# Performance work log

Hardware: AMD Instinct MI355X
Metric: run time of the kernel (lower is better)

The kernel has to match this reference:

```python
import jax, jax.numpy as jnp
import numpy as np
from jax import lax


def _lstm_layer(x, h0, c0, W_ih, W_hh, b_ih, b_hh):
    # x: [B,T,I]; precompute input projection for all timesteps: [B,T,4H]
    xg = jnp.einsum('bti,gi->btg', x, W_ih) + b_ih

    def step(carry, xg_t):
        h, c = carry
        gates = xg_t + h @ W_hh.T + b_hh  # [B,4H]
        i, f, g, o = jnp.split(gates, 4, axis=-1)  # PyTorch LSTMCell gate order
        i = jax.nn.sigmoid(i)
        f = jax.nn.sigmoid(f)
        g = jnp.tanh(g)
        o = jax.nn.sigmoid(o)
        c = f * c + i * g
        h = o * jnp.tanh(c)
        return (h, c), h

    (h, c), ys = lax.scan(step, (h0, c0), jnp.swapaxes(xg, 0, 1))  # scan over T
    return jnp.swapaxes(ys, 0, 1), h, c  # [B,T,H], [B,H], [B,H]


def setup_inputs() -> dict:
    key = jax.random.key(0)
    ks = jax.random.split(key, 10)
    B, T, I, H = 128, 256, 256, 1024
    s = 0.02
    return {
        'x': jax.random.normal(ks[0], (B, T, I), jnp.float32),
        'hx0': jnp.zeros((2, B, H), jnp.float32),
        'cx0': jnp.zeros((2, B, H), jnp.float32),
        'W_ih0': jax.random.normal(ks[1], (4 * H, I), jnp.float32) * s,
        'W_hh0': jax.random.normal(ks[2], (4 * H, H), jnp.float32) * s,
        'b_ih0': jax.random.normal(ks[3], (4 * H,), jnp.float32) * s,
        'b_hh0': jax.random.normal(ks[4], (4 * H,), jnp.float32) * s,
        'W_ih1': jax.random.normal(ks[5], (4 * H, H), jnp.float32) * s,
        'W_hh1': jax.random.normal(ks[6], (4 * H, H), jnp.float32) * s,
        'b_ih1': jax.random.normal(ks[7], (4 * H,), jnp.float32) * s,
        'b_hh1': jax.random.normal(ks[8], (4 * H,), jnp.float32) * s,
    }


def reference(x, hx0, cx0, W_ih0, W_hh0, b_ih0, b_hh0, W_ih1, W_hh1, b_ih1, b_hh1):
    # Eval mode / variational_inference=False with dropout=0.0: masks are exact ones.
    x, h, c = _lstm_layer(x, hx0[0], cx0[0], W_ih0, W_hh0, b_ih0, b_hh0)
    x, h, c = _lstm_layer(x, hx0[1], cx0[1], W_ih1, W_hh1, b_ih1, b_hh1)
    return x, h, c
```

## Files before the change

kernel.cpp:

```cpp
#include <hip/hip_runtime.h>

typedef __attribute__((ext_vector_type(8))) short short8;
typedef __attribute__((ext_vector_type(4))) float f32x4;

#define DEV static __device__ __forceinline__

DEV unsigned short f2b(float f) {
    union { float f; unsigned u; } v; v.f = f;
    unsigned r = (v.u + 0x7FFFu + ((v.u >> 16) & 1u)) >> 16;
    return (unsigned short)r;
}
DEV float b2f(unsigned short s) {
    union { unsigned u; float f; } v; v.u = ((unsigned)s) << 16;
    return v.f;
}
DEV float sigm(float x) { return 1.0f / (1.0f + __expf(-x)); }


__global__ void k_f2b(const float* __restrict__ src, unsigned short* __restrict__ dst, int n4) {
    int i = blockIdx.x * blockDim.x + threadIdx.x;
    if (i < n4) {
        float4 v = ((const float4*)src)[i];
        ushort4 o;
        o.x = f2b(v.x); o.y = f2b(v.y); o.z = f2b(v.z); o.w = f2b(v.w);
        ((ushort4*)dst)[i] = o;
    }
}

__global__ void k_perm(const float* __restrict__ src, unsigned short* __restrict__ dst, int Kq) {
    int i = blockIdx.x * blockDim.x + threadIdx.x;
    int total = 4096 * Kq;
    if (i >= total) return;
    int rp = i / Kq, kq = i - rp * Kq;
    int j = rp >> 2, g = rp & 3;
    float4 v = ((const float4*)src)[(size_t)(g * 1024 + j) * Kq + kq];
    ushort4 o;
    o.x = f2b(v.x); o.y = f2b(v.y); o.z = f2b(v.z); o.w = f2b(v.w);
    ((ushort4*)dst)[(size_t)rp * Kq + kq] = o;
}

__global__ void k_bias(const float* __restrict__ bi0, const float* __restrict__ bh0,
                       const float* __restrict__ bi1, const float* __restrict__ bh1,
                       float* __restrict__ d0, float* __restrict__ d1) {
    int i = blockIdx.x * blockDim.x + threadIdx.x;
    if (i < 4096) {
        int j = i >> 2, g = i & 3, s = g * 1024 + j;
        d0[i] = bi0[s] + bh0[s];
        d1[i] = bi1[s] + bh1[s];
    }
}

__global__ void k_init(const float* __restrict__ hx, const float* __restrict__ cx,
                       unsigned* __restrict__ hB0, unsigned* __restrict__ hB1,
                       float* __restrict__ c0, float* __restrict__ c1) {
    int i = blockIdx.x * blockDim.x + threadIdx.x;
    if (i < 128 * 512) {
        int b = i >> 9, j = i & 511;
        const float* p0 = hx + (size_t)b * 1024 + j * 2;
        const float* p1 = hx + 131072 + (size_t)b * 1024 + j * 2;
        hB0[i] = (unsigned)f2b(p0[0]) | ((unsigned)f2b(p0[1]) << 16);
        hB1[i] = (unsigned)f2b(p1[0]) | ((unsigned)f2b(p1[1]) << 16);
        c0[i * 2] = cx[i * 2];
        c0[i * 2 + 1] = cx[i * 2 + 1];
        c1[i * 2] = cx[131072 + i * 2];
        c1[i * 2 + 1] = cx[131072 + i * 2 + 1];
    }
}

__global__ __launch_bounds__(256) void k_gemm(
    const unsigned short* __restrict__ A, const unsigned short* __restrict__ W,
    unsigned short* __restrict__ out, int K, int t0, int TC) {
    __shared__ unsigned short ldsA[128 * 40];
    __shared__ unsigned short ldsB[128 * 40];
    const int tid = threadIdx.x;
    const int w = tid >> 6, l = tid & 63;
    const int wm = w >> 1, wn = w & 1;
    const int bm = blockIdx.x, bn = blockIdx.y;
    const int lr = l & 15, lk = (l >> 4) * 8;

    const int row0 = tid >> 2, inb = (tid & 3) << 4;
    const int row1 = row0 + 64;
    const int v0 = bm * 128 + row0, v1 = bm * 128 + row1;
    const size_t ar0 = (size_t)((v0 / TC) * 256 + t0 + (v0 % TC));
    const size_t ar1 = (size_t)((v1 / TC) * 256 + t0 + (v1 % TC));
    const size_t br0 = (size_t)(bn * 128 + row0);
    const size_t br1 = (size_t)(bn * 128 + row1);

    f32x4 acc[4][4];
#pragma unroll
    for (int a = 0; a < 4; a++)
#pragma unroll
        for (int b = 0; b < 4; b++) acc[a][b] = (f32x4){0.f, 0.f, 0.f, 0.f};

    for (int ks = 0; ks < K; ks += 32) {
        uint4 a0 = *(const uint4*)((const char*)A + (ar0 * K + ks) * 2 + inb);
        uint4 a1 = *(const uint4*)((const char*)A + (ar1 * K + ks) * 2 + inb);
        uint4 b0 = *(const uint4*)((const char*)W + (br0 * K + ks) * 2 + inb);
        uint4 b1 = *(const uint4*)((const char*)W + (br1 * K + ks) * 2 + inb);
        *(uint4*)((char*)ldsA + row0 * 80 + inb) = a0;
        *(uint4*)((char*)ldsA + row1 * 80 + inb) = a1;
        *(uint4*)((char*)ldsB + row0 * 80 + inb) = b0;
        *(uint4*)((char*)ldsB + row1 * 80 + inb) = b1;
        __syncthreads();
        short8 af[4], bf[4];
#pragma unroll
        for (int mt = 0; mt < 4; mt++)
            af[mt] = *(const short8*)((const char*)ldsA + (wm * 64 + mt * 16 + lr) * 80 + lk * 2);
#pragma unroll
        for (int nt = 0; nt < 4; nt++)
            bf[nt] = *(const short8*)((const char*)ldsB + (wn * 64 + nt * 16 + lr) * 80 + lk * 2);
#pragma unroll
        for (int mt = 0; mt < 4; mt++)
#pragma unroll
            for (int nt = 0; nt < 4; nt++)
                acc[mt][nt] = __builtin_amdgcn_mfma_f32_16x16x32_bf16(af[mt], bf[nt], acc[mt][nt], 0, 0, 0);
        __syncthreads();
    }

#pragma unroll
    for (int mt = 0; mt < 4; mt++)
#pragma unroll
        for (int nt = 0; nt < 4; nt++)
#pragma unroll
            for (int v4 = 0; v4 < 4; v4++) {
                int vr = bm * 128 + wm * 64 + mt * 16 + (l >> 4) * 4 + v4;
                int col = bn * 128 + wn * 64 + nt * 16 + lr;
                out[(size_t)vr * 4096 + col] = f2b(acc[mt][nt][v4]);
            }
}

template<int LAYER>
__global__ __launch_bounds__(512, 2) void k_lstm(
    const unsigned short* __restrict__ Wh,
    const unsigned short* __restrict__ xg,
    const float* __restrict__ bias,
    float* __restrict__ cbuf,
    unsigned* __restrict__ hA,
    unsigned* __restrict__ hB,
    unsigned short* __restrict__ y0,
    float* __restrict__ out,
    unsigned* __restrict__ flags,
    int t0, int TC)
{
    extern __shared__ char smem[];
    unsigned short* ldsW = (unsigned short*)smem;
    float* P0 = (float*)(smem + 64 * 2064);
    float* P1 = P0 + 16 * 132;
    float* P2 = P1 + 16 * 132;

    const int tid = threadIdx.x;
    const int g  = (int)blockIdx.x >> 5;
    const int nb = (int)blockIdx.x & 31;
    const int w  = tid >> 6;
    const int l  = tid & 63;
    const int lr = l & 15, lq = l >> 4;

    {
        const char* src = (const char*)(Wh + (size_t)nb * 128 * 1024);
#pragma unroll
        for (int it = 0; it < 16; it++) {
            int idx = it * 512 + tid;
            int row = idx >> 7, inr = (idx & 127) << 4;
            *(uint4*)(smem + row * 2064 + inr) = *(const uint4*)(src + (size_t)row * 2048 + inr);
        }
    }
    short8 wreg[16];
    {
        const unsigned short* src = Wh + (size_t)(nb * 128 + 64) * 1024 + w * 128;
#pragma unroll
        for (int ct = 0; ct < 4; ct++)
#pragma unroll
            for (int kk = 0; kk < 4; kk++)
                wreg[ct * 4 + kk] =
                    *(const short8*)(src + (size_t)(ct * 16 + lr) * 1024 + kk * 32 + lq * 8);
    }

    const int er = tid >> 4, ep = tid & 15;
    const int eb = g * 16 + (er & 15);
    const int ec0 = nb * 128 + ep * 8;
    const int eu0 = nb * 32 + ep * 2;
    float2 c2 = make_float2(0.f, 0.f);
    float4 bsA = make_float4(0.f, 0.f, 0.f, 0.f);
    float4 bsB = make_float4(0.f, 0.f, 0.f, 0.f);
    if (tid < 256) {
        c2 = *(const float2*)(cbuf + (size_t)eb * 1024 + eu0);
        bsA = *(const float4*)(bias + ec0);
        bsB = *(const float4*)(bias + ec0 + 4);
    }

    const size_t abase = (size_t)(g * 16 + lr) * 256 + (size_t)w * 32 + lq * 2;
    const char* wp = (const char*)ldsW + (size_t)lr * 2064 + w * 256 + lq * 16;

    const unsigned* fpw = flags + (size_t)(g * 32 + w * 4 + (l & 3)) * 16;
    unsigned* fmine = flags + (size_t)(g * 32 + nb) * 16;

    __syncthreads();

    for (int dt = 0; dt < TC; dt++) {
        const int t = t0 + dt;
        uint4 xv = make_uint4(0, 0, 0, 0);
        if (tid < 256)
            xv = *(const uint4*)(xg + (size_t)eb * ((size_t)TC * 4096) + (size_t)dt * 4096 + ec0);

        if (t > 0) {
            const unsigned tgt = (unsigned)t;
            while (!__all(__hip_atomic_load(fpw, __ATOMIC_RELAXED,
                                            __HIP_MEMORY_SCOPE_AGENT) >= tgt)) {}
        }

        const unsigned long long* ap =
            (const unsigned long long*)((t & 1) ? hA : hB) + abase;
        f32x4 acc[8];
#pragma unroll
        for (int i = 0; i < 8; i++) acc[i] = (f32x4){0.f, 0.f, 0.f, 0.f};
#pragma unroll
        for (int kk = 0; kk < 4; kk++) {
            union { unsigned long long u[2]; short8 s; } av;
            av.u[0] = __hip_atomic_load(ap + kk * 8,     __ATOMIC_RELAXED, __HIP_MEMORY_SCOPE_AGENT);
            av.u[1] = __hip_atomic_load(ap + kk * 8 + 1, __ATOMIC_RELAXED, __HIP_MEMORY_SCOPE_AGENT);
#pragma unroll
            for (int ct = 0; ct < 4; ct++) {
                short8 b = *(const short8*)(wp + (size_t)ct * 16 * 2064 + kk * 64);
                acc[ct] = __builtin_amdgcn_mfma_f32_16x16x32_bf16(av.s, b, acc[ct], 0, 0, 0);
            }
#pragma unroll
            for (int ct = 0; ct < 4; ct++)
                acc[4 + ct] = __builtin_amdgcn_mfma_f32_16x16x32_bf16(av.s, wreg[ct * 4 + kk], acc[4 + ct], 0, 0, 0);
        }

        if (w >= 5) {
            float* P = (w == 5) ? P0 : (w == 6) ? P1 : P2;
#pragma unroll
            for (int i = 0; i < 8; i++)
#pragma unroll
                for (int v = 0; v < 4; v++)
                    P[(lq * 4 + v) * 132 + i * 16 + lr] = acc[i][v];
        }
        __syncthreads();
        if (w >= 2 && w <= 4) {
            float* P = (w == 2) ? P0 : (w == 3) ? P1 : P2;
#pragma unroll
            for (int i = 0; i < 8; i++)
#pragma unroll
                for (int v = 0; v < 4; v++)
                    P[(lq * 4 + v) * 132 + i * 16 + lr] += acc[i][v];
        }
        __syncthreads();
        if (w < 2) {
            float* P = (w == 0) ? P0 : P1;
#pragma unroll
            for (int i = 0; i < 8; i++)
#pragma unroll
                for (int v = 0; v < 4; v++)
                    P[(lq * 4 + v) * 132 + i * 16 + lr] += acc[i][v];
        }
        __syncthreads();

        float h0v = 0.f, h1v = 0.f;
        if (tid < 256) {
            const float* pa = P0 + er * 132 + ep * 8;
            const float* pb = P1 + er * 132 + ep * 8;
            const float* pc = P2 + er * 132 + ep * 8;
            const unsigned short* xs = (const unsigned short*)&xv;
            float p0 = pa[0] + pb[0] + pc[0] + b2f(xs[0]) + bsA.x;
            float p1 = pa[1] + pb[1] + pc[1] + b2f(xs[1]) + bsA.y;
            float p2 = pa[2] + pb[2] + pc[2] + b2f(xs[2]) + bsA.z;
            float p3 = pa[3] + pb[3] + pc[3] + b2f(xs[3]) + bsA.w;
            float q0 = pa[4] + pb[4] + pc[4] + b2f(xs[4]) + bsB.x;
            float q1 = pa[5] + pb[5] + pc[5] + b2f(xs[5]) + bsB.y;
            float q2 = pa[6] + pb[6] + pc[6] + b2f(xs[6]) + bsB.z;
            float q3 = pa[7] + pb[7] + pc[7] + b2f(xs[7]) + bsB.w;
            float i0 = sigm(p0), f0 = sigm(p1), gv0 = tanhf(p2), o0 = sigm(p3);
            float i1 = sigm(q0), f1 = sigm(q1), gv1 = tanhf(q2), o1 = sigm(q3);
            c2.x = f0 * c2.x + i0 * gv0;
            c2.y = f1 * c2.y + i1 * gv1;
            h0v = o0 * tanhf(c2.x);
            h1v = o1 * tanhf(c2.y);
            unsigned hp = (unsigned)f2b(h0v) | ((unsigned)f2b(h1v) << 16);
            unsigned* hout = (t & 1) ? hB : hA;
            __hip_atomic_store(hout + (size_t)eb * 512 + eu0 / 2, hp,
                               __ATOMIC_RELAXED, __HIP_MEMORY_SCOPE_AGENT);
        }
        __syncthreads();
        if (tid == 0)
            __hip_atomic_store(fmine, (unsigned)(t + 1),
                               __ATOMIC_RELAXED, __HIP_MEMORY_SCOPE_AGENT);

        if (tid < 256) {
            if (LAYER == 0) {
                unsigned hp = (unsigned)f2b(h0v) | ((unsigned)f2b(h1v) << 16);
                ((unsigned*)y0)[((size_t)eb * 256 + t) * 512 + eu0 / 2] = hp;
            } else {
                *(float2*)(out + ((size_t)eb * 256 + t) * 1024 + eu0) = make_float2(h0v, h1v);
                if (t == 255) {
                    *(float2*)(out + (size_t)128 * 256 * 1024 + (size_t)eb * 1024 + eu0) =
                        make_float2(h0v, h1v);
                    *(float2*)(out + (size_t)128 * 256 * 1024 + (size_t)128 * 1024 + (size_t)eb * 1024 + eu0) =
                        make_float2(c2.x, c2.y);
                }
            }
        }
    }
    if (tid < 256)
        *(float2*)(cbuf + (size_t)eb * 1024 + eu0) = c2;
}


extern "C" void kernel_launch(void* const* d_in, const int* in_sizes, int n_in,
                              void* d_out, int out_size, void* d_ws, size_t ws_size,
                              hipStream_t stream) {
    const float* x    = (const float*)d_in[0];
    const float* hx0  = (const float*)d_in[1];
    const float* cx0  = (const float*)d_in[2];
    const float* Wih0 = (const float*)d_in[3];
    const float* Whh0 = (const float*)d_in[4];
    const float* bih0 = (const float*)d_in[5];
    const float* bhh0 = (const float*)d_in[6];
    const float* Wih1 = (const float*)d_in[7];
    const float* Whh1 = (const float*)d_in[8];
    const float* bih1 = (const float*)d_in[9];
    const float* bhh1 = (const float*)d_in[10];
    float* out = (float*)d_out;

    const int B = 128, T = 256, I = 256, H = 1024, G4 = 4096;
    const unsigned SMEM_BYTES = 64 * 2064 + 3 * 16 * 132 * 4;
    const int FLAGS_U32 = 8 * 32 * 16;

    hipFuncSetAttribute((const void*)&k_lstm<0>, hipFuncAttributeMaxDynamicSharedMemorySize, SMEM_BYTES);
    hipFuncSetAttribute((const void*)&k_lstm<1>, hipFuncAttributeMaxDynamicSharedMemorySize, SMEM_BYTES);

    char* p = (char*)d_ws;
    auto alloc = [&](size_t bytes) { char* r = p; p += (bytes + 255) & ~(size_t)255; return r; };
    unsigned short* xbf   = (unsigned short*)alloc((size_t)B * T * I * 2);
    unsigned short* Wih0p = (unsigned short*)alloc((size_t)G4 * I * 2);
    unsigned short* Whh0p = (unsigned short*)alloc((size_t)G4 * H * 2);
    unsigned short* Wih1p = (unsigned short*)alloc((size_t)G4 * H * 2);
    unsigned short* Whh1p = (unsigned short*)alloc((size_t)G4 * H * 2);
    float* bias0 = (float*)alloc(G4 * 4);
    float* bias1 = (float*)alloc(G4 * 4);
    unsigned short* y0 = (unsigned short*)alloc((size_t)B * T * H * 2);
    unsigned* hA0 = (unsigned*)alloc((size_t)B * 512 * 4);
    unsigned* hB0 = (unsigned*)alloc((size_t)B * 512 * 4);
    unsigned* hA1 = (unsigned*)alloc((size_t)B * 512 * 4);
    unsigned* hB1 = (unsigned*)alloc((size_t)B * 512 * 4);
    float* c0 = (float*)alloc((size_t)B * H * 4);
    float* c1 = (float*)alloc((size_t)B * H * 4);
    unsigned* flags0 = (unsigned*)alloc((size_t)2 * FLAGS_U32 * 4);
    unsigned* flags1 = flags0 + FLAGS_U32;
    size_t fixed = (size_t)(p - (char*)d_ws);
    int TC = 256;
    while (TC > 1 && fixed + (size_t)B * TC * G4 * 2 + 256 > ws_size) TC >>= 1;
    unsigned short* xg = (unsigned short*)alloc((size_t)B * TC * G4 * 2);

    hipMemsetAsync(flags0, 0, (size_t)2 * FLAGS_U32 * 4, stream);
    k_f2b<<<(B * T * I / 4 + 255) / 256, 256, 0, stream>>>(x, xbf, B * T * I / 4);
    k_perm<<<(G4 * (I / 4) + 255) / 256, 256, 0, stream>>>(Wih0, Wih0p, I / 4);
    k_perm<<<(G4 * (H / 4) + 255) / 256, 256, 0, stream>>>(Whh0, Whh0p, H / 4);
    k_perm<<<(G4 * (H / 4) + 255) / 256, 256, 0, stream>>>(Wih1, Wih1p, H / 4);
    k_perm<<<(G4 * (H / 4) + 255) / 256, 256, 0, stream>>>(Whh1, Whh1p, H / 4);
    k_bias<<<16, 256, 0, stream>>>(bih0, bhh0, bih1, bhh1, bias0, bias1);
    k_init<<<256, 256, 0, stream>>>(hx0, cx0, hB0, hB1, c0, c1);

    for (int t0 = 0; t0 < T; t0 += TC) {
        k_gemm<<<dim3(TC, 32), 256, 0, stream>>>(xbf, Wih0p, xg, I, t0, TC);
        int t0v = t0, TCv = TC;
        const unsigned short* Whp = Whh0p;
        const unsigned short* xgp = xg;
        const float* bp = bias0;
        float* cp = c0;
        unsigned* ha = hA0; unsigned* hb = hB0;
        unsigned short* y0p = y0;
        float* op = nullptr;
        unsigned* fl = flags0;
        void* args[] = {&Whp, &xgp, &bp, &cp, &ha, &hb, &y0p, &op, &fl, &t0v, &TCv};
        hipLaunchCooperativeKernel((const void*)&k_lstm<0>, dim3(256), dim3(512), args, SMEM_BYTES, stream);
    }
    for (int t0 = 0; t0 < T; t0 += TC) {
        k_gemm<<<dim3(TC, 32), 256, 0, stream>>>(y0, Wih1p, xg, H, t0, TC);
        int t0v = t0, TCv = TC;
        const unsigned short* Whp = Whh1p;
        const unsigned short* xgp = xg;
        const float* bp = bias1;
        float* cp = c1;
        unsigned* ha = hA1; unsigned* hb = hB1;
        unsigned short* y0p = nullptr;
        float* op = out;
        unsigned* fl = flags1;
        void* args[] = {&Whp, &xgp, &bp, &cp, &ha, &hb, &y0p, &op, &fl, &t0v, &TCv};
        hipLaunchCooperativeKernel((const void*)&k_lstm<1>, dim3(256), dim3(512), args, SMEM_BYTES, stream);
    }
}
```

Baseline: 3.046 ms.

## Fuse both LSTM layers into one cooperative kernel with wavefront pipelining

Replaces the two sequential per-layer recurrent kernels with one cooperative kernel. 128 workgroups run layer 0 and 128 run layer 1, which computes its input projection from layer-0 h on the fly, one timestep behind. This removes the layer-1 input GEMM, the y0 intermediate buffer and the serial second recurrent pass, overlapping the two recurrences. Each workgroup now handles 32 or 64 batch rows and half the SMs per layer. That raises per-step work and adds cross-layer flag dependencies that could lengthen each step.

```diff
diff --git a/kernel.cpp b/kernel.cpp
--- a/kernel.cpp
+++ b/kernel.cpp
@@ -15,6 +15,13 @@
     return v.f;
 }
 DEV float sigm(float x) { return 1.0f / (1.0f + __expf(-x)); }
+
+DEV unsigned long long ald(const unsigned long long* p) {
+    return __hip_atomic_load(p, __ATOMIC_RELAXED, __HIP_MEMORY_SCOPE_AGENT);
+}
+DEV unsigned aldu(const unsigned* p) {
+    return __hip_atomic_load(p, __ATOMIC_RELAXED, __HIP_MEMORY_SCOPE_AGENT);
+}
 
 
 __global__ void k_f2b(const float* __restrict__ src, unsigned short* __restrict__ dst, int n4) {
@@ -129,180 +136,349 @@
             }
 }
 
-template<int LAYER>
-__global__ __launch_bounds__(512, 2) void k_lstm(
-    const unsigned short* __restrict__ Wh,
+__global__ __launch_bounds__(512, 2) void k_fused(
+    const unsigned short* __restrict__ Wh0,
+    const unsigned short* __restrict__ Wi1,
+    const unsigned short* __restrict__ Wh1,
     const unsigned short* __restrict__ xg,
-    const float* __restrict__ bias,
-    float* __restrict__ cbuf,
-    unsigned* __restrict__ hA,
-    unsigned* __restrict__ hB,
-    unsigned short* __restrict__ y0,
+    const float* __restrict__ bias0,
+    const float* __restrict__ bias1,
+    float* __restrict__ c0buf, float* __restrict__ c1buf,
+    unsigned* __restrict__ h0A, unsigned* __restrict__ h0B,
+    unsigned* __restrict__ h1A, unsigned* __restrict__ h1B,
     float* __restrict__ out,
     unsigned* __restrict__ flags,
     int t0, int TC)
 {
     extern __shared__ char smem[];
-    unsigned short* ldsW = (unsigned short*)smem;
-    float* P0 = (float*)(smem + 64 * 2064);
-    float* P1 = P0 + 16 * 132;
-    float* P2 = P1 + 16 * 132;
-
+    char* ldsW = smem;
+    float* P0 = (float*)(smem + 48 * 2064);
+    const int wgid = (int)blockIdx.x;
     const int tid = threadIdx.x;
-    const int g  = (int)blockIdx.x >> 5;
-    const int nb = (int)blockIdx.x & 31;
-    const int w  = tid >> 6;
-    const int l  = tid & 63;
+    const int wv = tid >> 6;
+    const int l = tid & 63;
     const int lr = l & 15, lq = l >> 4;
 
-    {
-        const char* src = (const char*)(Wh + (size_t)nb * 128 * 1024);
-#pragma unroll
-        for (int it = 0; it < 16; it++) {
-            int idx = it * 512 + tid;
-            int row = idx >> 7, inr = (idx & 127) << 4;
-            *(uint4*)(smem + row * 2064 + inr) = *(const uint4*)(src + (size_t)row * 2048 + inr);
+    if (wgid < 128) {
+        const int g = wgid >> 5;
+        const int nb = wgid & 31;
+        float* P1 = P0 + 32 * 132;
+        float* P2 = P1 + 32 * 132;
+
+        {
+            const char* src = (const char*)(Wh0 + (size_t)nb * 128 * 1024);
+#pragma unroll
+            for (int it = 0; it < 12; it++) {
+                int idx = it * 512 + tid;
+                int row = idx >> 7, inr = (idx & 127) << 4;
+                *(uint4*)(ldsW + row * 2064 + inr) = *(const uint4*)(src + (size_t)row * 2048 + inr);
+            }
         }
+        short8 wreg[20];
+        {
+            const unsigned short* src = Wh0 + ((size_t)nb * 128 + 48) * 1024 + wv * 128;
+#pragma unroll
+            for (int ct = 0; ct < 5; ct++)
+#pragma unroll
+                for (int kk = 0; kk < 4; kk++)
+                    wreg[ct * 4 + kk] =
+                        *(const short8*)(src + (size_t)(ct * 16 + lr) * 1024 + kk * 32 + lq * 8);
+        }
+
+        const int er = tid >> 4, ep = tid & 15;
+        const int b0 = g * 32 + er;
+        const int ec0 = nb * 128 + ep * 8;
+        const int eu0 = nb * 32 + ep * 2;
+        float2 c2 = *(const float2*)(c0buf + (size_t)b0 * 1024 + eu0);
+        const float4 bsA = *(const float4*)(bias0 + ec0);
+        const float4 bsB = *(const float4*)(bias0 + ec0 + 4);
+
+        const size_t abase = (size_t)(g * 32 + lr) * 256 + (size_t)wv * 32 + lq * 2;
+        const char* wp = ldsW + (size_t)lr * 2064 + wv * 256 + lq * 16;
+
+        const unsigned* fA = flags + (size_t)(g * 32 + (l & 31)) * 16;
+        const unsigned* fB = flags + (size_t)(128 + (g >> 1) * 64 + l) * 16;
+        unsigned* fmine = flags + (size_t)(g * 32 + nb) * 16;
+
+        __syncthreads();
+
+        for (int dt = 0; dt < TC; dt++) {
+            const int t = t0 + dt;
+            uint4 xv = *(const uint4*)(xg + ((size_t)b0 * TC + dt) * 4096 + ec0);
+
+            if (t > 0) {
+                const unsigned tgt = (unsigned)t;
+                while (!__all((aldu(fA) >= tgt) & (aldu(fB) >= tgt - 1))) {}
+            }
+
+            const unsigned long long* ap =
+                (const unsigned long long*)((t & 1) ? h0A : h0B) + abase;
+            f32x4 acc[2][8];
+#pragma unroll
+            for (int i = 0; i < 2; i++)
+#pragma unroll
+                for (int j = 0; j < 8; j++) acc[i][j] = (f32x4){0.f, 0.f, 0.f, 0.f};
+#pragma unroll
+            for (int kk = 0; kk < 4; kk++) {
+                short8 bl0 = *(const short8*)(wp + 0 * 16 * 2064 + kk * 64);
+                short8 bl1 = *(const short8*)(wp + 1 * 16 * 2064 + kk * 64);
+                short8 bl2 = *(const short8*)(wp + 2 * 16 * 2064 + kk * 64);
+                union AV { unsigned long long u[2]; short8 s; } av0, av1;
+                av0.u[0] = ald(ap + kk * 8);
+                av0.u[1] = ald(ap + kk * 8 + 1);
+                acc[0][0] = __builtin_amdgcn_mfma_f32_16x16x32_bf16(av0.s, bl0, acc[0][0], 0, 0, 0);
+                acc[0][1] = __builtin_amdgcn_mfma_f32_16x16x32_bf16(av0.s, bl1, acc[0][1], 0, 0, 0);
+                acc[0][2] = __builtin_amdgcn_mfma_f32_16x16x32_bf16(av0.s, bl2, acc[0][2], 0, 0, 0);
+#pragma unroll
+                for (int ct = 0; ct < 5; ct++)
+                    acc[0][3 + ct] = __builtin_amdgcn_mfma_f32_16x16x32_bf16(av0.s, wreg[ct * 4 + kk], acc[0][3 + ct], 0, 0, 0);
+                av1.u[0] = ald(ap + 16 * 256 + kk * 8);
+                av1.u[1] = ald(ap + 16 * 256 + kk * 8 + 1);
+                acc[1][0] = __builtin_amdgcn_mfma_f32_16x16x32_bf16(av1.s, bl0, acc[1][0], 0, 0, 0);
+                acc[1][1] = __builtin_amdgcn_mfma_f32_16x16x32_bf16(av1.s, bl1, acc[1][1], 0, 0, 0);
+                acc[1][2] = __builtin_amdgcn_mfma_f32_16x16x32_bf16(av1.s, bl2, acc[1][2], 0, 0, 0);
+#pragma unroll
+                for (int ct = 0; ct < 5; ct++)
+                    acc[1][3 + ct] = __builtin_amdgcn_mfma_f32_16x16x32_bf16(av1.s, wreg[ct * 4 + kk], acc[1][3 + ct], 0, 0, 0);
+            }
+
+            if (wv >= 5) {
+                float* P = (wv == 5) ? P0 : (wv == 6) ? P1 : P2;
+#pragma unroll
+                for (int rt = 0; rt < 2; rt++)
+#pragma unroll
+                    for (int j = 0; j < 8; j++)
+#pragma unroll
+                        for (int v = 0; v < 4; v++)
+                            P[(rt * 16 + lq * 4 + v) * 132 + j * 16 + lr] = acc[rt][j][v];
+            }
+            __syncthreads();
+            if (wv >= 2 && wv <= 4) {
+                float* P = (wv == 2) ? P0 : (wv == 3) ? P1 : P2;
+#pragma unroll
+                for (int rt = 0; rt < 2; rt++)
+#pragma unroll
+                    for (int j = 0; j < 8; j++)
+#pragma unroll
+                        for (int v = 0; v < 4; v++)
+                            P[(rt * 16 + lq * 4 + v) * 132 + j * 16 + lr] += acc[rt][j][v];
+            }
+            __syncthreads();
+            if (wv < 2) {
+                float* P = (wv == 0) ? P0 : P1;
+#pragma unroll
+                for (int rt = 0; rt < 2; rt++)
+#pragma unroll
+                    for (int j = 0; j < 8; j++)
+#pragma unroll
+                        for (int v = 0; v < 4; v++)
+                            P[(rt * 16 + lq * 4 + v) * 132 + j * 16 + lr] += acc[rt][j][v];
+            }
+            __syncthreads();
+
+            {
+                const float* pa = P0 + er * 132 + ep * 8;
+                const float* pb = P1 + er * 132 + ep * 8;
+                const float* pc = P2 + er * 132 + ep * 8;
+                const unsigned short* xs = (const unsigned short*)&xv;
+                float p0 = pa[0] + pb[0] + pc[0] + b2f(xs[0]) + bsA.x;
+                float p1 = pa[1] + pb[1] + pc[1] + b2f(xs[1]) + bsA.y;
+                float p2 = pa[2] + pb[2] + pc[2] + b2f(xs[2]) + bsA.z;
+                float p3 = pa[3] + pb[3] + pc[3] + b2f(xs[3]) + bsA.w;
+                float q0 = pa[4] + pb[4] + pc[4] + b2f(xs[4]) + bsB.x;
+                float q1 = pa[5] + pb[5] + pc[5] + b2f(xs[5]) + bsB.y;
+                float q2 = pa[6] + pb[6] + pc[6] + b2f(xs[6]) + bsB.z;
+                float q3 = pa[7] + pb[7] + pc[7] + b2f(xs[7]) + bsB.w;
+                float i0 = sigm(p0), f0 = sigm(p1), gv0 = tanhf(p2), o0 = sigm(p3);
+                float i1 = sigm(q0), f1 = sigm(q1), gv1 = tanhf(q2), o1 = sigm(q3);
+                c2.x = f0 * c2.x + i0 * gv0;
+                c2.y = f1 * c2.y + i1 * gv1;
+                float h0v = o0 * tanhf(c2.x);
+                float h1v = o1 * tanhf(c2.y);
+                unsigned hp = (unsigned)f2b(h0v) | ((unsigned)f2b(h1v) << 16);
+                unsigned* hout = (t & 1) ? h0B : h0A;
+                __hip_atomic_store(hout + (size_t)b0 * 512 + nb * 16 + ep, hp,
+                                   __ATOMIC_RELAXED, __HIP_MEMORY_SCOPE_AGENT);
+            }
+            __syncthreads();
+            if (tid == 0)
+                __hip_atomic_store(fmine, (unsigned)(t + 1),
+                                   __ATOMIC_RELAXED, __HIP_MEMORY_SCOPE_AGENT);
+        }
+        *(float2*)(c0buf + (size_t)b0 * 1024 + eu0) = c2;
+    } else {
+        const int w1 = wgid - 128;
+        const int g = w1 >> 6;
+        const int n = w1 & 63;
+        float* P1 = P0 + 64 * 68;
+        float* P2 = P1 + 64 * 68;
+
+        {
+#pragma unroll
+            for (int it = 0; it < 12; it++) {
+                int idx = it * 512 + tid;
+                int row = idx >> 7, inr = (idx & 127) << 4;
+                const char* src = (row < 32)
+                    ? (const char*)(Wi1 + (size_t)(n * 64 + row) * 1024)
+                    : (const char*)(Wh1 + (size_t)(n * 64 + row - 32) * 1024);
+                *(uint4*)(ldsW + row * 2064 + inr) = *(const uint4*)(src + inr);
+            }
+        }
+        short8 wreg[24];
+        {
+            if (wv < 4) {
+                const unsigned short* src = Wi1 + ((size_t)n * 64 + 32) * 1024 + wv * 256;
+#pragma unroll
+                for (int ct = 0; ct < 2; ct++)
+#pragma unroll
+                    for (int kk = 0; kk < 8; kk++)
+                        wreg[ct * 8 + kk] =
+                            *(const short8*)(src + (size_t)(ct * 16 + lr) * 1024 + kk * 32 + lq * 8);
+            } else {
+                const unsigned short* src = Wh1 + ((size_t)n * 64 + 16) * 1024 + (wv - 4) * 256;
+#pragma unroll
+                for (int ct = 0; ct < 3; ct++)
+#pragma unroll
+                    for (int kk = 0; kk < 8; kk++)
+                        wreg[ct * 8 + kk] =
+                            *(const short8*)(src + (size_t)(ct * 16 + lr) * 1024 + kk * 32 + lq * 8);
+            }
+        }
+
+        const int er2 = tid >> 3, up = tid & 7;
+        const int b1 = g * 64 + er2;
+        const int ec = n * 64 + up * 8;
+        const int u0 = n * 16 + up * 2;
+        float2 c2 = *(const float2*)(c1buf + (size_t)b1 * 1024 + u0);
+        const float4 bsA = *(const float4*)(bias1 + ec);
+        const float4 bsB = *(const float4*)(bias1 + ec + 4);
+
+        const size_t abase = (size_t)(g * 64 + lr) * 256 + (size_t)(wv & 3) * 64 + lq * 2;
+        const char* wpl = (wv < 4)
+            ? (ldsW + (size_t)lr * 2064 + wv * 512 + lq * 16)
+            : (ldsW + (size_t)(32 + lr) * 2064 + (wv - 4) * 512 + lq * 16);
+
+        const unsigned* fA = flags + (size_t)(g * 64 + l) * 16;
+        const unsigned* fB = flags + (size_t)(128 + g * 64 + l) * 16;
+        unsigned* fmine = flags + (size_t)(128 + g * 64 + n) * 16;
+
+        __syncthreads();
+
+        for (int dt = 0; dt < TC; dt++) {
+            const int t = t0 + dt;
+
+            {
+                const unsigned tgt = (unsigned)t;
+                while (!__all((aldu(fA) >= tgt + 1) & (aldu(fB) >= tgt))) {}
+            }
+
+            const unsigned long long* ap = (wv < 4)
+                ? ((const unsigned long long*)((t & 1) ? h0B : h0A) + abase)
+                : ((const unsigned long long*)((t & 1) ? h1A : h1B) + abase);
+            f32x4 acc[4][4];
+#pragma unroll
+            for (int i = 0; i < 4; i++)
+#pragma unroll
+                for (int j = 0; j < 4; j++) acc[i][j] = (f32x4){0.f, 0.f, 0.f, 0.f};
+#pragma unroll
+            for (int kk = 0; kk < 8; kk++) {
+                short8 bl[4];
+                if (wv < 4) {
+                    bl[0] = *(const short8*)(wpl + 0 * 16 * 2064 + kk * 64);
+                    bl[1] = *(const short8*)(wpl + 1 * 16 * 2064 + kk * 64);
+                    bl[2] = wreg[0 * 8 + kk];
+                    bl[3] = wreg[1 * 8 + kk];
+                } else {
+                    bl[0] = *(const short8*)(wpl + kk * 64);
+                    bl[1] = wreg[0 * 8 + kk];
+                    bl[2] = wreg[1 * 8 + kk];
+                    bl[3] = wreg[2 * 8 + kk];
+                }
+#pragma unroll
+                for (int rt = 0; rt < 4; rt++) {
+                    union AV { unsigned long long u[2]; short8 s; } av;
+                    av.u[0] = ald(ap + (size_t)rt * 4096 + kk * 8);
+                    av.u[1] = ald(ap + (size_t)rt * 4096 + kk * 8 + 1);
+                    acc[rt][0] = __builtin_amdgcn_mfma_f32_16x16x32_bf16(av.s, bl[0], acc[rt][0], 0, 0, 0);
+                    acc[rt][1] = __builtin_amdgcn_mfma_f32_16x16x32_bf16(av.s, bl[1], acc[rt][1], 0, 0, 0);
+                    acc[rt][2] = __builtin_amdgcn_mfma_f32_16x16x32_bf16(av.s, bl[2], acc[rt][2], 0, 0, 0);
+                    acc[rt][3] = __builtin_amdgcn_mfma_f32_16x16x32_bf16(av.s, bl[3], acc[rt][3], 0, 0, 0);
+                }
+            }
+
+            if (wv >= 5) {
+                float* P = (wv == 5) ? P0 : (wv == 6) ? P1 : P2;
+#pragma unroll
+                for (int rt = 0; rt < 4; rt++)
+#pragma unroll
+                    for (int j = 0; j < 4; j++)
+#pragma unroll
+                        for (int v = 0; v < 4; v++)
+                            P[(rt * 16 + lq * 4 + v) * 68 + j * 16 + lr] = acc[rt][j][v];
+            }
+            __syncthreads();
+            if (wv >= 2 && wv <= 4) {
+                float* P = (wv == 2) ? P0 : (wv == 3) ? P1 : P2;
+#pragma unroll
+                for (int rt = 0; rt < 4; rt++)
+#pragma unroll
+                    for (int j = 0; j < 4; j++)
+#pragma unroll
+                        for (int v = 0; v < 4; v++)
+                            P[(rt * 16 + lq * 4 + v) * 68 + j * 16 + lr] += acc[rt][j][v];
+            }
+            __syncthreads();
+            if (wv < 2) {
+                float* P = (wv == 0) ? P0 : P1;
+#pragma unroll
+                for (int rt = 0; rt < 4; rt++)
+#pragma unroll
+                    for (int j = 0; j < 4; j++)
+#pragma unroll
+                        for (int v = 0; v < 4; v++)
+                            P[(rt * 16 + lq * 4 + v) * 68 + j * 16 + lr] += acc[rt][j][v];
+            }
+            __syncthreads();
+
+            float h0v, h1v;
+            {
+                const float* pa = P0 + er2 * 68 + up * 8;
+                const float* pb = P1 + er2 * 68 + up * 8;
+                const float* pc = P2 + er2 * 68 + up * 8;
+                float p0 = pa[0] + pb[0] + pc[0] + bsA.x;
+                float p1 = pa[1] + pb[1] + pc[1] + bsA.y;
+                float p2 = pa[2] + pb[2] + pc[2] + bsA.z;
+                float p3 = pa[3] + pb[3] + pc[3] + bsA.w;
+                float q0 = pa[4] + pb[4] + pc[4] + bsB.x;
+                float q1 = pa[5] + pb[5] + pc[5] + bsB.y;
+                float q2 = pa[6] + pb[6] + pc[6] + bsB.z;
+                float q3 = pa[7] + pb[7] + pc[7] + bsB.w;
+                float i0 = sigm(p0), f0 = sigm(p1), gv0 = tanhf(p2), o0 = sigm(p3);
+                float i1 = sigm(q0), f1 = sigm(q1), gv1 = tanhf(q2), o1 = sigm(q3);
+                c2.x = f0 * c2.x + i0 * gv0;
+                c2.y = f1 * c2.y + i1 * gv1;
+                h0v = o0 * tanhf(c2.x);
+                h1v = o1 * tanhf(c2.y);
+                unsigned hp = (unsigned)f2b(h0v) | ((unsigned)f2b(h1v) << 16);
+                unsigned* hout = (t & 1) ? h1B : h1A;
+                __hip_atomic_store(hout + (size_t)b1 * 512 + n * 8 + up, hp,
+                                   __ATOMIC_RELAXED, __HIP_MEMORY_SCOPE_AGENT);
+            }
+            __syncthreads();
+            if (tid == 0)
+                __hip_atomic_store(fmine, (unsigned)(t + 1),
+                                   __ATOMIC_RELAXED, __HIP_MEMORY_SCOPE_AGENT);
+
+            *(float2*)(out + ((size_t)b1 * 256 + t) * 1024 + u0) = make_float2(h0v, h1v);
+            if (t == 255) {
+                *(float2*)(out + (size_t)128 * 256 * 1024 + (size_t)b1 * 1024 + u0) =
+                    make_float2(h0v, h1v);
+                *(float2*)(out + (size_t)128 * 256 * 1024 + (size_t)128 * 1024 + (size_t)b1 * 1024 + u0) =
+                    make_float2(c2.x, c2.y);
+            }
+        }
+        *(float2*)(c1buf + (size_t)b1 * 1024 + u0) = c2;
     }
-    short8 wreg[16];
-    {
-        const unsigned short* src = Wh + (size_t)(nb * 128 + 64) * 1024 + w * 128;
-#pragma unroll
-        for (int ct = 0; ct < 4; ct++)
-#pragma unroll
-            for (int kk = 0; kk < 4; kk++)
-                wreg[ct * 4 + kk] =
-                    *(const short8*)(src + (size_t)(ct * 16 + lr) * 1024 + kk * 32 + lq * 8);
-    }
-
-    const int er = tid >> 4, ep = tid & 15;
-    const int eb = g * 16 + (er & 15);
-    const int ec0 = nb * 128 + ep * 8;
-    const int eu0 = nb * 32 + ep * 2;
-    float2 c2 = make_float2(0.f, 0.f);
-    float4 bsA = make_float4(0.f, 0.f, 0.f, 0.f);
-    float4 bsB = make_float4(0.f, 0.f, 0.f, 0.f);
-    if (tid < 256) {
-        c2 = *(const float2*)(cbuf + (size_t)eb * 1024 + eu0);
-        bsA = *(const float4*)(bias + ec0);
-        bsB = *(const float4*)(bias + ec0 + 4);
-    }
-
-    const size_t abase = (size_t)(g * 16 + lr) * 256 + (size_t)w * 32 + lq * 2;
-    const char* wp = (const char*)ldsW + (size_t)lr * 2064 + w * 256 + lq * 16;
-
-    const unsigned* fpw = flags + (size_t)(g * 32 + w * 4 + (l & 3)) * 16;
-    unsigned* fmine = flags + (size_t)(g * 32 + nb) * 16;
-
-    __syncthreads();
-
-    for (int dt = 0; dt < TC; dt++) {
-        const int t = t0 + dt;
-        uint4 xv = make_uint4(0, 0, 0, 0);
-        if (tid < 256)
-            xv = *(const uint4*)(xg + (size_t)eb * ((size_t)TC * 4096) + (size_t)dt * 4096 + ec0);
-
-        if (t > 0) {
-            const unsigned tgt = (unsigned)t;
-            while (!__all(__hip_atomic_load(fpw, __ATOMIC_RELAXED,
-                                            __HIP_MEMORY_SCOPE_AGENT) >= tgt)) {}
-        }
-
-        const unsigned long long* ap =
-            (const unsigned long long*)((t & 1) ? hA : hB) + abase;
-        f32x4 acc[8];
-#pragma unroll
-        for (int i = 0; i < 8; i++) acc[i] = (f32x4){0.f, 0.f, 0.f, 0.f};
-#pragma unroll
-        for (int kk = 0; kk < 4; kk++) {
-            union { unsigned long long u[2]; short8 s; } av;
-            av.u[0] = __hip_atomic_load(ap + kk * 8,     __ATOMIC_RELAXED, __HIP_MEMORY_SCOPE_AGENT);
-            av.u[1] = __hip_atomic_load(ap + kk * 8 + 1, __ATOMIC_RELAXED, __HIP_MEMORY_SCOPE_AGENT);
-#pragma unroll
-            for (int ct = 0; ct < 4; ct++) {
-                short8 b = *(const short8*)(wp + (size_t)ct * 16 * 2064 + kk * 64);
-                acc[ct] = __builtin_amdgcn_mfma_f32_16x16x32_bf16(av.s, b, acc[ct], 0, 0, 0);
-            }
-#pragma unroll
-            for (int ct = 0; ct < 4; ct++)
-                acc[4 + ct] = __builtin_amdgcn_mfma_f32_16x16x32_bf16(av.s, wreg[ct * 4 + kk], acc[4 + ct], 0, 0, 0);
-        }
-
-        if (w >= 5) {
-            float* P = (w == 5) ? P0 : (w == 6) ? P1 : P2;
-#pragma unroll
-            for (int i = 0; i < 8; i++)
-#pragma unroll
-                for (int v = 0; v < 4; v++)
-                    P[(lq * 4 + v) * 132 + i * 16 + lr] = acc[i][v];
-        }
-        __syncthreads();
-        if (w >= 2 && w <= 4) {
-            float* P = (w == 2) ? P0 : (w == 3) ? P1 : P2;
-#pragma unroll
-            for (int i = 0; i < 8; i++)
-#pragma unroll
-                for (int v = 0; v < 4; v++)
-                    P[(lq * 4 + v) * 132 + i * 16 + lr] += acc[i][v];
-        }
-        __syncthreads();
-        if (w < 2) {
-            float* P = (w == 0) ? P0 : P1;
-#pragma unroll
-            for (int i = 0; i < 8; i++)
-#pragma unroll
-                for (int v = 0; v < 4; v++)
-                    P[(lq * 4 + v) * 132 + i * 16 + lr] += acc[i][v];
-        }
-        __syncthreads();
-
-        float h0v = 0.f, h1v = 0.f;
-        if (tid < 256) {
-            const float* pa = P0 + er * 132 + ep * 8;
-            const float* pb = P1 + er * 132 + ep * 8;
-            const float* pc = P2 + er * 132 + ep * 8;
-            const unsigned short* xs = (const unsigned short*)&xv;
-            float p0 = pa[0] + pb[0] + pc[0] + b2f(xs[0]) + bsA.x;
-            float p1 = pa[1] + pb[1] + pc[1] + b2f(xs[1]) + bsA.y;
-            float p2 = pa[2] + pb[2] + pc[2] + b2f(xs[2]) + bsA.z;
-            float p3 = pa[3] + pb[3] + pc[3] + b2f(xs[3]) + bsA.w;
-            float q0 = pa[4] + pb[4] + pc[4] + b2f(xs[4]) + bsB.x;
-            float q1 = pa[5] + pb[5] + pc[5] + b2f(xs[5]) + bsB.y;
-            float q2 = pa[6] + pb[6] + pc[6] + b2f(xs[6]) + bsB.z;
-            float q3 = pa[7] + pb[7] + pc[7] + b2f(xs[7]) + bsB.w;
-            float i0 = sigm(p0), f0 = sigm(p1), gv0 = tanhf(p2), o0 = sigm(p3);
-            float i1 = sigm(q0), f1 = sigm(q1), gv1 = tanhf(q2), o1 = sigm(q3);
-            c2.x = f0 * c2.x + i0 * gv0;
-            c2.y = f1 * c2.y + i1 * gv1;
-            h0v = o0 * tanhf(c2.x);
-            h1v = o1 * tanhf(c2.y);
-            unsigned hp = (unsigned)f2b(h0v) | ((unsigned)f2b(h1v) << 16);
-            unsigned* hout = (t & 1) ? hB : hA;
-            __hip_atomic_store(hout + (size_t)eb * 512 + eu0 / 2, hp,
-                               __ATOMIC_RELAXED, __HIP_MEMORY_SCOPE_AGENT);
-        }
-        __syncthreads();
-        if (tid == 0)
-            __hip_atomic_store(fmine, (unsigned)(t + 1),
-                               __ATOMIC_RELAXED, __HIP_MEMORY_SCOPE_AGENT);
-
-        if (tid < 256) {
-            if (LAYER == 0) {
-                unsigned hp = (unsigned)f2b(h0v) | ((unsigned)f2b(h1v) << 16);
-                ((unsigned*)y0)[((size_t)eb * 256 + t) * 512 + eu0 / 2] = hp;
-            } else {
-                *(float2*)(out + ((size_t)eb * 256 + t) * 1024 + eu0) = make_float2(h0v, h1v);
-                if (t == 255) {
-                    *(float2*)(out + (size_t)128 * 256 * 1024 + (size_t)eb * 1024 + eu0) =
-                        make_float2(h0v, h1v);
-                    *(float2*)(out + (size_t)128 * 256 * 1024 + (size_t)128 * 1024 + (size_t)eb * 1024 + eu0) =
-                        make_float2(c2.x, c2.y);
-                }
-            }
-        }
-    }
-    if (tid < 256)
-        *(float2*)(cbuf + (size_t)eb * 1024 + eu0) = c2;
 }
 
 
@@ -323,11 +499,9 @@
     float* out = (float*)d_out;
 
     const int B = 128, T = 256, I = 256, H = 1024, G4 = 4096;
-    const unsigned SMEM_BYTES = 64 * 2064 + 3 * 16 * 132 * 4;
-    const int FLAGS_U32 = 8 * 32 * 16;
-
-    hipFuncSetAttribute((const void*)&k_lstm<0>, hipFuncAttributeMaxDynamicSharedMemorySize, SMEM_BYTES);
-    hipFuncSetAttribute((const void*)&k_lstm<1>, hipFuncAttributeMaxDynamicSharedMemorySize, SMEM_BYTES);
+    const unsigned SMEM_BYTES = 48 * 2064 + 3 * 64 * 68 * 4;
+
+    hipFuncSetAttribute((const void*)&k_fused, hipFuncAttributeMaxDynamicSharedMemorySize, SMEM_BYTES);
 
     char* p = (char*)d_ws;
     auto alloc = [&](size_t bytes) { char* r = p; p += (bytes + 255) & ~(size_t)255; return r; };
@@ -338,21 +512,19 @@
     unsigned short* Whh1p = (unsigned short*)alloc((size_t)G4 * H * 2);
     float* bias0 = (float*)alloc(G4 * 4);
     float* bias1 = (float*)alloc(G4 * 4);
-    unsigned short* y0 = (unsigned short*)alloc((size_t)B * T * H * 2);
     unsigned* hA0 = (unsigned*)alloc((size_t)B * 512 * 4);
     unsigned* hB0 = (unsigned*)alloc((size_t)B * 512 * 4);
     unsigned* hA1 = (unsigned*)alloc((size_t)B * 512 * 4);
     unsigned* hB1 = (unsigned*)alloc((size_t)B * 512 * 4);
     float* c0 = (float*)alloc((size_t)B * H * 4);
     float* c1 = (float*)alloc((size_t)B * H * 4);
-    unsigned* flags0 = (unsigned*)alloc((size_t)2 * FLAGS_U32 * 4);
-    unsigned* flags1 = flags0 + FLAGS_U32;
+    unsigned* flags = (unsigned*)alloc((size_t)256 * 16 * 4);
     size_t fixed = (size_t)(p - (char*)d_ws);
     int TC = 256;
     while (TC > 1 && fixed + (size_t)B * TC * G4 * 2 + 256 > ws_size) TC >>= 1;
     unsigned short* xg = (unsigned short*)alloc((size_t)B * TC * G4 * 2);
 
-    hipMemsetAsync(flags0, 0, (size_t)2 * FLAGS_U32 * 4, stream);
+    hipMemsetAsync(flags, 0, (size_t)256 * 16 * 4, stream);
     k_f2b<<<(B * T * I / 4 + 255) / 256, 256, 0, stream>>>(x, xbf, B * T * I / 4);
     k_perm<<<(G4 * (I / 4) + 255) / 256, 256, 0, stream>>>(Wih0, Wih0p, I / 4);
     k_perm<<<(G4 * (H / 4) + 255) / 256, 256, 0, stream>>>(Whh0, Whh0p, H / 4);
@@ -364,29 +536,19 @@
     for (int t0 = 0; t0 < T; t0 += TC) {
         k_gemm<<<dim3(TC, 32), 256, 0, stream>>>(xbf, Wih0p, xg, I, t0, TC);
         int t0v = t0, TCv = TC;
-        const unsigned short* Whp = Whh0p;
+        const unsigned short* wh0 = Whh0p;
+        const unsigned short* wi1 = Wih1p;
+        const unsigned short* wh1 = Whh1p;
         const unsigned short* xgp = xg;
-        const float* bp = bias0;
-        float* cp = c0;
-        unsigned* ha = hA0; unsigned* hb = hB0;
-        unsigned short* y0p = y0;
-        float* op = nullptr;
-        unsigned* fl = flags0;
-        void* args[] = {&Whp, &xgp, &bp, &cp, &ha, &hb, &y0p, &op, &fl, &t0v, &TCv};
-        hipLaunchCooperativeKernel((const void*)&k_lstm<0>, dim3(256), dim3(512), args, SMEM_BYTES, stream);
+        const float* b0p = bias0;
+        const float* b1p = bias1;
+        float* c0p = c0; float* c1p = c1;
+        unsigned* h0a = hA0; unsigned* h0b = hB0;
+        unsigned* h1a = hA1; unsigned* h1b = hB1;
+        float* op = out;
+        unsigned* fl = flags;
+        void* args[] = {&wh0, &wi1, &wh1, &xgp, &b0p, &b1p, &c0p, &c1p,
+                        &h0a, &h0b, &h1a, &h1b, &op, &fl, &t0v, &TCv};
+        hipLaunchCooperativeKernel((const void*)&k_fused, dim3(256), dim3(512), args, SMEM_BYTES, stream);
     }
-    for (int t0 = 0; t0 < T; t0 += TC) {
-        k_gemm<<<dim3(TC, 32), 256, 0, stream>>>(y0, Wih1p, xg, H, t0, TC);
-        int t0v = t0, TCv = TC;
-        const unsigned short* Whp = Whh1p;
-        const unsigned short* xgp = xg;
-        const float* bp = bias1;
-        float* cp = c1;
-        unsigned* ha = hA1; unsigned* hb = hB1;
-        unsigned short* y0p = nullptr;
-        float* op = out;
-        unsigned* fl = flags1;
-        void* args[] = {&Whp, &xgp, &bp, &cp, &ha, &hb, &y0p, &op, &fl, &t0v, &TCv};
-        hipLaunchCooperativeKernel((const void*)&k_lstm<1>, dim3(256), dim3(512), args, SMEM_BYTES, stream);
-    }
-}
+}
```

Measured after the change: 4.994 ms. 1.64x slower.

## Fuse input projection into recurrent LSTM kernel with register-resident input weights

Applied to the files above, without the earlier changes.

Removes the separate input-projection GEMM and its bf16 xg intermediate buffer. Each recurrent step now computes the x·W_ih contribution inside the persistent LSTM kernel, with W_ih slices held in registers (8 or 32 short8 per lane) and input rows read directly. The flag wait is also changed so each lane polls one of 32 block flags. This avoids the GEMM launches and the xg write/read traffic, but it adds MFMA work and global loads to the serial critical path of every timestep and raises register pressure, especially for layer 1 with K=1024.

```diff
diff --git a/kernel.cpp b/kernel.cpp
--- a/kernel.cpp
+++ b/kernel.cpp
@@ -67,83 +67,21 @@
     }
 }
 
-__global__ __launch_bounds__(256) void k_gemm(
-    const unsigned short* __restrict__ A, const unsigned short* __restrict__ W,
-    unsigned short* __restrict__ out, int K, int t0, int TC) {
-    __shared__ unsigned short ldsA[128 * 40];
-    __shared__ unsigned short ldsB[128 * 40];
-    const int tid = threadIdx.x;
-    const int w = tid >> 6, l = tid & 63;
-    const int wm = w >> 1, wn = w & 1;
-    const int bm = blockIdx.x, bn = blockIdx.y;
-    const int lr = l & 15, lk = (l >> 4) * 8;
-
-    const int row0 = tid >> 2, inb = (tid & 3) << 4;
-    const int row1 = row0 + 64;
-    const int v0 = bm * 128 + row0, v1 = bm * 128 + row1;
-    const size_t ar0 = (size_t)((v0 / TC) * 256 + t0 + (v0 % TC));
-    const size_t ar1 = (size_t)((v1 / TC) * 256 + t0 + (v1 % TC));
-    const size_t br0 = (size_t)(bn * 128 + row0);
-    const size_t br1 = (size_t)(bn * 128 + row1);
-
-    f32x4 acc[4][4];
-#pragma unroll
-    for (int a = 0; a < 4; a++)
-#pragma unroll
-        for (int b = 0; b < 4; b++) acc[a][b] = (f32x4){0.f, 0.f, 0.f, 0.f};
-
-    for (int ks = 0; ks < K; ks += 32) {
-        uint4 a0 = *(const uint4*)((const char*)A + (ar0 * K + ks) * 2 + inb);
-        uint4 a1 = *(const uint4*)((const char*)A + (ar1 * K + ks) * 2 + inb);
-        uint4 b0 = *(const uint4*)((const char*)W + (br0 * K + ks) * 2 + inb);
-        uint4 b1 = *(const uint4*)((const char*)W + (br1 * K + ks) * 2 + inb);
-        *(uint4*)((char*)ldsA + row0 * 80 + inb) = a0;
-        *(uint4*)((char*)ldsA + row1 * 80 + inb) = a1;
-        *(uint4*)((char*)ldsB + row0 * 80 + inb) = b0;
-        *(uint4*)((char*)ldsB + row1 * 80 + inb) = b1;
-        __syncthreads();
-        short8 af[4], bf[4];
-#pragma unroll
-        for (int mt = 0; mt < 4; mt++)
-            af[mt] = *(const short8*)((const char*)ldsA + (wm * 64 + mt * 16 + lr) * 80 + lk * 2);
-#pragma unroll
-        for (int nt = 0; nt < 4; nt++)
-            bf[nt] = *(const short8*)((const char*)ldsB + (wn * 64 + nt * 16 + lr) * 80 + lk * 2);
-#pragma unroll
-        for (int mt = 0; mt < 4; mt++)
-#pragma unroll
-            for (int nt = 0; nt < 4; nt++)
-                acc[mt][nt] = __builtin_amdgcn_mfma_f32_16x16x32_bf16(af[mt], bf[nt], acc[mt][nt], 0, 0, 0);
-        __syncthreads();
-    }
-
-#pragma unroll
-    for (int mt = 0; mt < 4; mt++)
-#pragma unroll
-        for (int nt = 0; nt < 4; nt++)
-#pragma unroll
-            for (int v4 = 0; v4 < 4; v4++) {
-                int vr = bm * 128 + wm * 64 + mt * 16 + (l >> 4) * 4 + v4;
-                int col = bn * 128 + wn * 64 + nt * 16 + lr;
-                out[(size_t)vr * 4096 + col] = f2b(acc[mt][nt][v4]);
-            }
-}
-
-template<int LAYER>
+template<int LAYER, int KI, int XI>
 __global__ __launch_bounds__(512, 2) void k_lstm(
     const unsigned short* __restrict__ Wh,
-    const unsigned short* __restrict__ xg,
+    const unsigned short* __restrict__ Wi,
+    const unsigned short* __restrict__ xin,
     const float* __restrict__ bias,
     float* __restrict__ cbuf,
     unsigned* __restrict__ hA,
     unsigned* __restrict__ hB,
     unsigned short* __restrict__ y0,
     float* __restrict__ out,
-    unsigned* __restrict__ flags,
-    int t0, int TC)
+    unsigned* __restrict__ flags)
 {
     extern __shared__ char smem[];
-    unsigned short* ldsW = (unsigned short*)smem;
+    char* ldsW = smem;
     float* P0 = (float*)(smem + 64 * 2064);
     float* P1 = P0 + 16 * 132;
     float* P2 = P1 + 16 * 132;
@@ -151,7 +89,7 @@
     const int tid = threadIdx.x;
     const int g  = (int)blockIdx.x >> 5;
     const int nb = (int)blockIdx.x & 31;
-    const int w  = tid >> 6;
+    const int wv = tid >> 6;
     const int l  = tid & 63;
     const int lr = l & 15, lq = l >> 4;
 
@@ -161,18 +99,27 @@
         for (int it = 0; it < 16; it++) {
             int idx = it * 512 + tid;
             int row = idx >> 7, inr = (idx & 127) << 4;
-            *(uint4*)(smem + row * 2064 + inr) = *(const uint4*)(src + (size_t)row * 2048 + inr);
+            *(uint4*)(ldsW + row * 2064 + inr) = *(const uint4*)(src + (size_t)row * 2048 + inr);
         }
     }
     short8 wreg[16];
     {
-        const unsigned short* src = Wh + (size_t)(nb * 128 + 64) * 1024 + w * 128;
+        const unsigned short* src = Wh + (size_t)(nb * 128 + 64) * 1024 + wv * 128;
 #pragma unroll
         for (int ct = 0; ct < 4; ct++)
 #pragma unroll
             for (int kk = 0; kk < 4; kk++)
                 wreg[ct * 4 + kk] =
                     *(const short8*)(src + (size_t)(ct * 16 + lr) * 1024 + kk * 32 + lq * 8);
+    }
+    short8 wregi[8 * XI];
+    {
+#pragma unroll
+        for (int j = 0; j < 8; j++)
+#pragma unroll
+            for (int kk = 0; kk < XI; kk++)
+                wregi[j * XI + kk] = *(const short8*)(
+                    Wi + (size_t)(nb * 128 + j * 16 + lr) * KI + wv * (KI / 8) + kk * 32 + lq * 8);
     }
 
     const int er = tid >> 4, ep = tid & 15;
@@ -188,23 +135,19 @@
         bsB = *(const float4*)(bias + ec0 + 4);
     }
 
-    const size_t abase = (size_t)(g * 16 + lr) * 256 + (size_t)w * 32 + lq * 2;
-    const char* wp = (const char*)ldsW + (size_t)lr * 2064 + w * 256 + lq * 16;
-
-    const unsigned* fpw = flags + (size_t)(g * 32 + w * 4 + (l & 3)) * 16;
+    const size_t abase = (size_t)(g * 16 + lr) * 256 + (size_t)wv * 32 + lq * 2;
+    const char* wp = ldsW + (size_t)lr * 2064 + wv * 256 + lq * 16;
+    const unsigned short* xrow = xin + (size_t)(g * 16 + lr) * 256 * KI + wv * (KI / 8) + lq * 8;
+
+    const unsigned* fp = flags + (size_t)(g * 32 + (l & 31)) * 16;
     unsigned* fmine = flags + (size_t)(g * 32 + nb) * 16;
 
     __syncthreads();
 
-    for (int dt = 0; dt < TC; dt++) {
-        const int t = t0 + dt;
-        uint4 xv = make_uint4(0, 0, 0, 0);
-        if (tid < 256)
-            xv = *(const uint4*)(xg + (size_t)eb * ((size_t)TC * 4096) + (size_t)dt * 4096 + ec0);
-
+    for (int t = 0; t < 256; t++) {
         if (t > 0) {
             const unsigned tgt = (unsigned)t;
-            while (!__all(__hip_atomic_load(fpw, __ATOMIC_RELAXED,
+            while (!__all(__hip_atomic_load(fp, __ATOMIC_RELAXED,
                                             __HIP_MEMORY_SCOPE_AGENT) >= tgt)) {}
         }
 
@@ -227,9 +170,19 @@
             for (int ct = 0; ct < 4; ct++)
                 acc[4 + ct] = __builtin_amdgcn_mfma_f32_16x16x32_bf16(av.s, wreg[ct * 4 + kk], acc[4 + ct], 0, 0, 0);
         }
-
-        if (w >= 5) {
-            float* P = (w == 5) ? P0 : (w == 6) ? P1 : P2;
+        {
+            const unsigned short* xt = xrow + (size_t)t * KI;
+#pragma unroll
+            for (int kk = 0; kk < XI; kk++) {
+                short8 ax = *(const short8*)(xt + kk * 32);
+#pragma unroll
+                for (int j = 0; j < 8; j++)
+                    acc[j] = __builtin_amdgcn_mfma_f32_16x16x32_bf16(ax, wregi[j * XI + kk], acc[j], 0, 0, 0);
+            }
+        }
+
+        if (wv >= 5) {
+            float* P = (wv == 5) ? P0 : (wv == 6) ? P1 : P2;
 #pragma unroll
             for (int i = 0; i < 8; i++)
 #pragma unroll
@@ -237,8 +190,8 @@
                     P[(lq * 4 + v) * 132 + i * 16 + lr] = acc[i][v];
         }
         __syncthreads();
-        if (w >= 2 && w <= 4) {
-            float* P = (w == 2) ? P0 : (w == 3) ? P1 : P2;
+        if (wv >= 2 && wv <= 4) {
+            float* P = (wv == 2) ? P0 : (wv == 3) ? P1 : P2;
 #pragma unroll
             for (int i = 0; i < 8; i++)
 #pragma unroll
@@ -246,8 +199,8 @@
                     P[(lq * 4 + v) * 132 + i * 16 + lr] += acc[i][v];
         }
         __syncthreads();
-        if (w < 2) {
-            float* P = (w == 0) ? P0 : P1;
+        if (wv < 2) {
+            float* P = (wv == 0) ? P0 : P1;
 #pragma unroll
             for (int i = 0; i < 8; i++)
 #pragma unroll
@@ -261,15 +214,14 @@
             const float* pa = P0 + er * 132 + ep * 8;
             const float* pb = P1 + er * 132 + ep * 8;
             const float* pc = P2 + er * 132 + ep * 8;
-            const unsigned short* xs = (const unsigned short*)&xv;
-            float p0 = pa[0] + pb[0] + pc[0] + b2f(xs[0]) + bsA.x;
-            float p1 = pa[1] + pb[1] + pc[1] + b2f(xs[1]) + bsA.y;
-            float p2 = pa[2] + pb[2] + pc[2] + b2f(xs[2]) + bsA.z;
-            float p3 = pa[3] + pb[3] + pc[3] + b2f(xs[3]) + bsA.w;
-            float q0 = pa[4] + pb[4] + pc[4] + b2f(xs[4]) + bsB.x;
-            float q1 = pa[5] + pb[5] + pc[5] + b2f(xs[5]) + bsB.y;
-            float q2 = pa[6] + pb[6] + pc[6] + b2f(xs[6]) + bsB.z;
-            float q3 = pa[7] + pb[7] + pc[7] + b2f(xs[7]) + bsB.w;
+            float p0 = pa[0] + pb[0] + pc[0] + bsA.x;
+            float p1 = pa[1] + pb[1] + pc[1] + bsA.y;
+            float p2 = pa[2] + pb[2] + pc[2] + bsA.z;
+            float p3 = pa[3] + pb[3] + pc[3] + bsA.w;
+            float q0 = pa[4] + pb[4] + pc[4] + bsB.x;
+            float q1 = pa[5] + pb[5] + pc[5] + bsB.y;
+            float q2 = pa[6] + pb[6] + pc[6] + bsB.z;
+            float q3 = pa[7] + pb[7] + pc[7] + bsB.w;
             float i0 = sigm(p0), f0 = sigm(p1), gv0 = tanhf(p2), o0 = sigm(p3);
             float i1 = sigm(q0), f1 = sigm(q1), gv1 = tanhf(q2), o1 = sigm(q3);
             c2.x = f0 * c2.x + i0 * gv0;
@@ -326,8 +278,8 @@
     const unsigned SMEM_BYTES = 64 * 2064 + 3 * 16 * 132 * 4;
     const int FLAGS_U32 = 8 * 32 * 16;
 
-    hipFuncSetAttribute((const void*)&k_lstm<0>, hipFuncAttributeMaxDynamicSharedMemorySize, SMEM_BYTES);
-    hipFuncSetAttribute((const void*)&k_lstm<1>, hipFuncAttributeMaxDynamicSharedMemorySize, SMEM_BYTES);
+    hipFuncSetAttribute((const void*)&k_lstm<0, 256, 1>, hipFuncAttributeMaxDynamicSharedMemorySize, SMEM_BYTES);
+    hipFuncSetAttribute((const void*)&k_lstm<1, 1024, 4>, hipFuncAttributeMaxDynamicSharedMemorySize, SMEM_BYTES);
 
     char* p = (char*)d_ws;
     auto alloc = [&](size_t bytes) { char* r = p; p += (bytes + 255) & ~(size_t)255; return r; };
@@ -347,10 +299,6 @@
     float* c1 = (float*)alloc((size_t)B * H * 4);
     unsigned* flags0 = (unsigned*)alloc((size_t)2 * FLAGS_U32 * 4);
     unsigned* flags1 = flags0 + FLAGS_U32;
-    size_t fixed = (size_t)(p - (char*)d_ws);
-    int TC = 256;
-    while (TC > 1 && fixed + (size_t)B * TC * G4 * 2 + 256 > ws_size) TC >>= 1;
-    unsigned short* xg = (unsigned short*)alloc((size_t)B * TC * G4 * 2);
 
     hipMemsetAsync(flags0, 0, (size_t)2 * FLAGS_U32 * 4, stream);
     k_f2b<<<(B * T * I / 4 + 255) / 256, 256, 0, stream>>>(x, xbf, B * T * I / 4);
@@ -361,32 +309,30 @@
     k_bias<<<16, 256, 0, stream>>>(bih0, bhh0, bih1, bhh1, bias0, bias1);
     k_init<<<256, 256, 0, stream>>>(hx0, cx0, hB0, hB1, c0, c1);
 
-    for (int t0 = 0; t0 < T; t0 += TC) {
-        k_gemm<<<dim3(TC, 32), 256, 0, stream>>>(xbf, Wih0p, xg, I, t0, TC);
-        int t0v = t0, TCv = TC;
+    {
         const unsigned short* Whp = Whh0p;
-        const unsigned short* xgp = xg;
+        const unsigned short* Wip = Wih0p;
+        const unsigned short* xp = xbf;
         const float* bp = bias0;
         float* cp = c0;
         unsigned* ha = hA0; unsigned* hb = hB0;
         unsigned short* y0p = y0;
         float* op = nullptr;
         unsigned* fl = flags0;
-        void* args[] = {&Whp, &xgp, &bp, &cp, &ha, &hb, &y0p, &op, &fl, &t0v, &TCv};
-        hipLaunchCooperativeKernel((const void*)&k_lstm<0>, dim3(256), dim3(512), args, SMEM_BYTES, stream);
-    }
-    for (int t0 = 0; t0 < T; t0 += TC) {
-        k_gemm<<<dim3(TC, 32), 256, 0, stream>>>(y0, Wih1p, xg, H, t0, TC);
-        int t0v = t0, TCv = TC;
+        void* args[] = {&Whp, &Wip, &xp, &bp, &cp, &ha, &hb, &y0p, &op, &fl};
+        hipLaunchCooperativeKernel((const void*)&k_lstm<0, 256, 1>, dim3(256), dim3(512), args, SMEM_BYTES, stream);
+    }
+    {
         const unsigned short* Whp = Whh1p;
-        const unsigned short* xgp = xg;
+        const unsigned short* Wip = Wih1p;
+        const unsigned short* xp = y0;
         const float* bp = bias1;
         float* cp = c1;
         unsigned* ha = hA1; unsigned* hb = hB1;
         unsigned short* y0p = nullptr;
         float* op = out;
         unsigned* fl = flags1;
-        void* args[] = {&Whp, &xgp, &bp, &cp, &ha, &hb, &y0p, &op, &fl, &t0v, &TCv};
-        hipLaunchCooperativeKernel((const void*)&k_lstm<1>, dim3(256), dim3(512), args, SMEM_BYTES, stream);
-    }
-}
+        void* args[] = {&Whp, &Wip, &xp, &bp, &cp, &ha, &hb, &y0p, &op, &fl};
+        hipLaunchCooperativeKernel((const void*)&k_lstm<1, 1024, 4>, dim3(256), dim3(512), args, SMEM_BYTES, stream);
+    }
+}
```

Result: slower. 3.311 ms (+8.7%).
